# Kernel optimization log

Hardware: AMD Instinct MI355X
Metric: run time of the kernel (lower is better)

## Reference

```python
import jax, jax.numpy as jnp
import numpy as np

B, S, D = 1, 2048, 4096
N_Q, N_KV, HD = 32, 8, 128
N_REP = N_Q // N_KV
WINDOW = 1024
NEG = -1e9


def setup_inputs() -> dict:
    key = jax.random.key(0)
    ks = jax.random.split(key, 6)
    x = jax.random.normal(ks[0], (B, S, D), dtype=jnp.float32)
    # RoPE frequencies (Llama-style): theta = 10000^{-2i/HD}
    inv_freq = 1.0 / (10000.0 ** (np.arange(0, HD, 2, dtype=np.float32) / HD))
    t = np.arange(S, dtype=np.float32)
    ang = np.outer(t, inv_freq)  # [S, HD//2]
    freqs_cos = jnp.asarray(np.cos(ang), dtype=jnp.float32)
    freqs_sin = jnp.asarray(np.sin(ang), dtype=jnp.float32)
    # additive causal mask [S, S]: 0 on/below diag, -1e9 above
    mask = jnp.where(jnp.tril(jnp.ones((S, S), dtype=bool)), 0.0, NEG).astype(jnp.float32)
    scale = 0.02
    w_q = jax.random.normal(ks[1], (D, N_Q * HD), dtype=jnp.float32) * scale
    w_k = jax.random.normal(ks[2], (D, N_KV * HD), dtype=jnp.float32) * scale
    w_v = jax.random.normal(ks[3], (D, N_KV * HD), dtype=jnp.float32) * scale
    w_o = jax.random.normal(ks[4], (N_Q * HD, D), dtype=jnp.float32) * scale
    return {"x": x, "freqs_cos": freqs_cos, "freqs_sin": freqs_sin, "mask": mask,
            "w_q": w_q, "w_k": w_k, "w_v": w_v, "w_o": w_o}


def _rope(t, cos, sin):
    # t: [B, S, H, HD]; cos/sin: [S, HD//2] -> complex multiply on pairs
    tp = t.reshape(*t.shape[:-1], HD // 2, 2)
    e, o = tp[..., 0], tp[..., 1]
    c = cos[None, :, None, :]
    s = sin[None, :, None, :]
    re = e * c - o * s
    ro = e * s + o * c
    return jnp.stack([re, ro], axis=-1).reshape(t.shape)


def reference(x, freqs_cos, freqs_sin, mask, w_q, w_k, w_v, w_o):
    b, s, _ = x.shape
    xq = (x @ w_q).reshape(b, s, N_Q, HD)
    xk = (x @ w_k).reshape(b, s, N_KV, HD)
    xv = (x @ w_v).reshape(b, s, N_KV, HD)
    xq = _rope(xq, freqs_cos, freqs_sin)
    xk = _rope(xk, freqs_cos, freqs_sin)
    # GQA head repeat
    keys = jnp.repeat(xk, N_REP, axis=2)    # [b, s, N_Q, HD]
    values = jnp.repeat(xv, N_REP, axis=2)
    q = xq.transpose(0, 2, 1, 3)            # [b, h, s, hd]
    k = keys.transpose(0, 2, 1, 3)
    v = values.transpose(0, 2, 1, 3)
    scores = jnp.einsum('bhqd,bhkd->bhqk', q, k) / jnp.sqrt(jnp.float32(HD))
    scores = scores + mask[None, None, :, :]
    # sliding-window band: attend only to keys within WINDOW positions back
    idx = jnp.arange(s)
    diff = idx[:, None] - idx[None, :]
    sliding = (diff >= 0) & (diff < WINDOW)
    scores = jnp.where(sliding[None, None, :, :], scores, NEG)
    probs = jax.nn.softmax(scores, axis=-1).astype(q.dtype)
    out = jnp.einsum('bhqk,bhkd->bhqd', probs, v)
    out = out.transpose(0, 2, 1, 3).reshape(b, s, N_Q * HD)
    return out @ w_o
```

## Files before the change

### kernel.cpp

```cpp
#include <hip/hip_runtime.h>

typedef unsigned short u16;
typedef unsigned int u32;
typedef __bf16 bf16x8 __attribute__((ext_vector_type(8)));
typedef __bf16 bf16x4 __attribute__((ext_vector_type(4)));
typedef float f32x4 __attribute__((ext_vector_type(4)));

#define MFMA16(a, b, c) __builtin_amdgcn_mfma_f32_16x16x32_bf16(a, b, c, 0, 0, 0)

__device__ __forceinline__ u16 f2bf(float f) {
  u32 u = __float_as_uint(f);
  u += 0x7FFFu + ((u >> 16) & 1u);
  return (u16)(u >> 16);
}
__device__ __forceinline__ float bf2f(u16 h) {
  return __uint_as_float(((u32)h) << 16);
}

__device__ __forceinline__ void gload_lds16(const u16* g, u16* l) {
  __builtin_amdgcn_global_load_lds((__attribute__((address_space(1))) void*)g,
                                   (__attribute__((address_space(3))) void*)l,
                                   16, 0, 0);
}

__global__ __launch_bounds__(256) void cvt_x(const float* __restrict__ in,
                                             u16* __restrict__ out) {
  int i = (blockIdx.x * 256 + threadIdx.x) * 4;
  float4 v = *(const float4*)&in[i];
  ushort4 o;
  o.x = f2bf(v.x);
  o.y = f2bf(v.y);
  o.z = f2bf(v.z);
  o.w = f2bf(v.w);
  *(ushort4*)&out[i] = o;
}

__global__ __launch_bounds__(256) void tbf_f2b(const float* __restrict__ in,
                                               u16* __restrict__ out,
                                               int ldin, int ldout) {
  __shared__ float tile[64][65];
  const int t = threadIdx.x;
  const int c4 = t & 15;
  const int rb = t >> 4;
  const int r0 = blockIdx.y * 64;
  const int c0 = blockIdx.x * 64;
#pragma unroll
  for (int p = 0; p < 4; p++) {
    int r = p * 16 + rb;
    float4 v = *(const float4*)&in[(size_t)(r0 + r) * ldin + c0 + c4 * 4];
    tile[r][c4 * 4 + 0] = v.x;
    tile[r][c4 * 4 + 1] = v.y;
    tile[r][c4 * 4 + 2] = v.z;
    tile[r][c4 * 4 + 3] = v.w;
  }
  __syncthreads();
#pragma unroll
  for (int p = 0; p < 4; p++) {
    int oc = p * 16 + rb;
    ushort4 v;
    v.x = f2bf(tile[c4 * 4 + 0][oc]);
    v.y = f2bf(tile[c4 * 4 + 1][oc]);
    v.z = f2bf(tile[c4 * 4 + 2][oc]);
    v.w = f2bf(tile[c4 * 4 + 3][oc]);
    *(ushort4*)&out[(size_t)(c0 + oc) * ldout + r0 + c4 * 4] = v;
  }
}

__global__ __launch_bounds__(256) void tbf_b(const u16* __restrict__ in,
                                             u16* __restrict__ out,
                                             int ldin, int ldout) {
  __shared__ u16 tile[64][68];
  const int t = threadIdx.x;
  const int c4 = t & 15;
  const int rb = t >> 4;
  const int r0 = blockIdx.y * 64;
  const int c0 = blockIdx.x * 64;
#pragma unroll
  for (int p = 0; p < 4; p++) {
    int r = p * 16 + rb;
    ushort4 v = *(const ushort4*)&in[(size_t)(r0 + r) * ldin + c0 + c4 * 4];
    *(ushort4*)&tile[r][c4 * 4] = v;
  }
  __syncthreads();
#pragma unroll
  for (int p = 0; p < 4; p++) {
    int oc = p * 16 + rb;
    ushort4 v;
    v.x = tile[c4 * 4 + 0][oc];
    v.y = tile[c4 * 4 + 1][oc];
    v.z = tile[c4 * 4 + 2][oc];
    v.w = tile[c4 * 4 + 3][oc];
    *(ushort4*)&out[(size_t)(c0 + oc) * ldout + r0 + c4 * 4] = v;
  }
}

__global__ __launch_bounds__(256) void gemm_bt(
    const u16* __restrict__ A, const u16* __restrict__ B1,
    const u16* __restrict__ B2, const u16* __restrict__ B3,
    void* __restrict__ Cv, int K, int ldc, int n1, int n12, int f32out) {
  __shared__ __attribute__((aligned(16))) u16 AsS[128 * 32];
  __shared__ __attribute__((aligned(16))) u16 BsS[128 * 32];
  const int tid = threadIdx.x;
  const int wave = tid >> 6;
  const int lane = tid & 63;
  const int l16 = lane & 15;
  const int quad = lane >> 4;
  const int bm = blockIdx.y * 128;
  const int bn0 = blockIdx.x * 128;

  const u16* Bp;
  int bnl;
  if (bn0 < n1) { Bp = B1; bnl = bn0; }
  else if (bn0 < n12) { Bp = B2; bnl = bn0 - n1; }
  else { Bp = B3; bnl = bn0 - n12; }

  const int chunk = wave * 2;
  const int srow = chunk * 16 + (lane >> 2);
  const int skq = (lane & 3) * 8;
  const u16* gA0 = A + (size_t)(bm + srow) * K + skq;
  const u16* gB0 = Bp + (size_t)(bnl + srow) * K + skq;
  u16* lA0 = &AsS[chunk * 512];
  u16* lB0 = &BsS[chunk * 512];
  const size_t k16 = (size_t)16 * K;

  f32x4 acc[4][4];
#pragma unroll
  for (int i = 0; i < 4; i++)
#pragma unroll
    for (int j = 0; j < 4; j++) acc[i][j] = (f32x4){0.f, 0.f, 0.f, 0.f};

  const int wr = (wave >> 1) * 64;
  const int wc = (wave & 1) * 64;

  for (int k0 = 0; k0 < K; k0 += 32) {
    __syncthreads();
    gload_lds16(gA0 + k0, lA0);
    gload_lds16(gA0 + k0 + k16, lA0 + 512);
    gload_lds16(gB0 + k0, lB0);
    gload_lds16(gB0 + k0 + k16, lB0 + 512);
    __syncthreads();
    bf16x8 af[4], bfr[4];
#pragma unroll
    for (int i = 0; i < 4; i++)
      af[i] = *(const bf16x8*)&AsS[(wr + i * 16 + l16) * 32 + quad * 8];
#pragma unroll
    for (int j = 0; j < 4; j++)
      bfr[j] = *(const bf16x8*)&BsS[(wc + j * 16 + l16) * 32 + quad * 8];
#pragma unroll
    for (int i = 0; i < 4; i++)
#pragma unroll
      for (int j = 0; j < 4; j++)
        acc[i][j] = MFMA16(af[i], bfr[j], acc[i][j]);
  }
  if (f32out) {
    float* C = (float*)Cv;
#pragma unroll
    for (int i = 0; i < 4; i++)
#pragma unroll
      for (int j = 0; j < 4; j++)
#pragma unroll
        for (int r = 0; r < 4; r++) {
          int row = bm + wr + i * 16 + quad * 4 + r;
          int col = bn0 + wc + j * 16 + l16;
          C[(size_t)row * ldc + col] = acc[i][j][r];
        }
  } else {
    u16* C = (u16*)Cv;
#pragma unroll
    for (int i = 0; i < 4; i++)
#pragma unroll
      for (int j = 0; j < 4; j++)
#pragma unroll
        for (int r = 0; r < 4; r++) {
          int row = bm + wr + i * 16 + quad * 4 + r;
          int col = bn0 + wc + j * 16 + l16;
          C[(size_t)row * ldc + col] = f2bf(acc[i][j][r]);
        }
  }
}

__global__ __launch_bounds__(256) void rope_k(u16* __restrict__ qkv,
                                              const float* __restrict__ fc,
                                              const float* __restrict__ fs) {
  int idx = blockIdx.x * 256 + threadIdx.x;
  int j = idx & 63;
  int rem = idx >> 6;
  int head = rem % 40;
  int s = rem / 40;
  float c = fc[s * 64 + j];
  float sn = fs[s * 64 + j];
  int col = (head < 32) ? (head * 128 + 2 * j) : (4096 + (head - 32) * 128 + 2 * j);
  u32* p = (u32*)&qkv[(size_t)s * 6144 + col];
  u32 v = *p;
  float e = bf2f((u16)(v & 0xFFFFu));
  float o = bf2f((u16)(v >> 16));
  float re = e * c - o * sn;
  float ro = e * sn + o * c;
  *p = (u32)f2bf(re) | ((u32)f2bf(ro) << 16);
}

__global__ __launch_bounds__(256) void attn_k(const u16* __restrict__ qkv,
                                              const u16* __restrict__ vt,
                                              u16* __restrict__ outb) {
  __shared__ __attribute__((aligned(16))) u16 Kb[2][32 * 128];
  __shared__ __attribute__((aligned(16))) u16 Vb[2][128 * 32];
  __shared__ __attribute__((aligned(16))) u16 plds[4][32 * 36];
  const int h = blockIdx.x;
  const int q0 = blockIdx.y * 128;
  const int t = threadIdx.x;
  const int wave = t >> 6;
  const int lane = t & 63;
  const int l16 = lane & 15;
  const int quad = lane >> 4;
  const int hkv = h >> 2;
  const int qw = q0 + wave * 32;
  u16* myp = &plds[wave][0];

  bf16x8 qa[2][4];
#pragma unroll
  for (int i = 0; i < 2; i++)
#pragma unroll
    for (int kc = 0; kc < 4; kc++)
      qa[i][kc] = *(const bf16x8*)&qkv[(size_t)(qw + i * 16 + l16) * 6144 +
                                       h * 128 + kc * 32 + quad * 8];

  f32x4 o[2][8];
#pragma unroll
  for (int i = 0; i < 2; i++)
#pragma unroll
    for (int d = 0; d < 8; d++) o[i][d] = (f32x4){0.f, 0.f, 0.f, 0.f};
  float lloc[2][4] = {{0.f, 0.f, 0.f, 0.f}, {0.f, 0.f, 0.f, 0.f}};

  const int kb_start = (q0 - 1023 > 0 ? q0 - 1023 : 0) & ~31;
  const int kb_last = q0 + 96;
  const float sc = 0.08838834764831845f;

  const int kr0 = t >> 4, kc0s = t & 15;
  const int kr1 = (256 + t) >> 4, kc1s = t & 15;
  const int vr0 = t >> 2, vc0s = t & 3;
  const int vr1 = (256 + t) >> 2, vc1s = t & 3;
  const u16* kg = qkv + 4096 + hkv * 128;
  const u16* vg = vt + (size_t)hkv * 128 * 2048;

#define STAGE(kb_, nb_)                                                        \
  do {                                                                         \
    int kb__ = (kb_);                                                          \
    gload_lds16(&kg[(size_t)(kb__ + kr0) * 6144 + (kc0s ^ (kr0 & 15)) * 8],    \
                &Kb[nb_][t * 8]);                                              \
    gload_lds16(&kg[(size_t)(kb__ + kr1) * 6144 + (kc1s ^ (kr1 & 15)) * 8],    \
                &Kb[nb_][2048 + t * 8]);                                       \
    gload_lds16(&vg[(size_t)vr0 * 2048 + kb__ + (vc0s ^ (vr0 & 3)) * 8],       \
                &Vb[nb_][t * 8]);                                              \
    gload_lds16(&vg[(size_t)vr1 * 2048 + kb__ + (vc1s ^ (vr1 & 3)) * 8],       \
                &Vb[nb_][2048 + t * 8]);                                       \
  } while (0)

  STAGE(kb_start, 0);
  int cur = 0;

  for (int kb = kb_start; kb <= kb_last; kb += 32) {
    __syncthreads();
    if (kb + 32 <= kb_last) STAGE(kb + 32, cur ^ 1);
    const u16* kcur = &Kb[cur][0];
    const u16* vcur = &Vb[cur][0];

    f32x4 s0[2] = {(f32x4){0.f, 0.f, 0.f, 0.f}, (f32x4){0.f, 0.f, 0.f, 0.f}};
    f32x4 s1[2] = {(f32x4){0.f, 0.f, 0.f, 0.f}, (f32x4){0.f, 0.f, 0.f, 0.f}};
#pragma unroll
    for (int kc = 0; kc < 4; kc++) {
      int ch = ((kc * 4 + quad) ^ l16) * 8;
      bf16x8 b0 = *(const bf16x8*)&kcur[l16 * 128 + ch];
      bf16x8 b1 = *(const bf16x8*)&kcur[(l16 + 16) * 128 + ch];
      s0[0] = MFMA16(qa[0][kc], b0, s0[0]);
      s1[0] = MFMA16(qa[0][kc], b1, s1[0]);
      s0[1] = MFMA16(qa[1][kc], b0, s0[1]);
      s1[1] = MFMA16(qa[1][kc], b1, s1[1]);
    }

    float p0[2][4], p1[2][4];
    bool fast = (kb + 31 <= qw) && (qw + 31 - kb <= 1023);
    if (fast) {
#pragma unroll
      for (int i = 0; i < 2; i++)
#pragma unroll
        for (int r = 0; r < 4; r++) {
          p0[i][r] = __expf(s0[i][r] * sc);
          p1[i][r] = __expf(s1[i][r] * sc);
        }
    } else {
#pragma unroll
      for (int i = 0; i < 2; i++)
#pragma unroll
        for (int r = 0; r < 4; r++) {
          int row = qw + i * 16 + quad * 4 + r;
          int col0 = kb + l16;
          int col1 = col0 + 16;
          bool v0 = (col0 <= row) && (row - col0 < 1024);
          bool v1 = (col1 <= row) && (row - col1 < 1024);
          p0[i][r] = v0 ? __expf(s0[i][r] * sc) : 0.f;
          p1[i][r] = v1 ? __expf(s1[i][r] * sc) : 0.f;
        }
    }
#pragma unroll
    for (int i = 0; i < 2; i++)
#pragma unroll
      for (int r = 0; r < 4; r++) {
        lloc[i][r] += p0[i][r] + p1[i][r];
        myp[(i * 16 + quad * 4 + r) * 36 + l16] = f2bf(p0[i][r]);
        myp[(i * 16 + quad * 4 + r) * 36 + l16 + 16] = f2bf(p1[i][r]);
      }
    asm volatile("s_waitcnt lgkmcnt(0)" ::: "memory");
    bf16x8 pa[2];
#pragma unroll
    for (int i = 0; i < 2; i++) {
      bf16x4 lo = *(const bf16x4*)&myp[(i * 16 + l16) * 36 + quad * 8];
      bf16x4 hi = *(const bf16x4*)&myp[(i * 16 + l16) * 36 + quad * 8 + 4];
#pragma unroll
      for (int j = 0; j < 4; j++) {
        pa[i][j] = lo[j];
        pa[i][j + 4] = hi[j];
      }
    }
#pragma unroll
    for (int d = 0; d < 8; d++) {
      int rv = l16 + 16 * d;
      bf16x8 vb = *(const bf16x8*)&vcur[rv * 32 + ((quad ^ (l16 & 3)) * 8)];
      o[0][d] = MFMA16(pa[0], vb, o[0][d]);
      o[1][d] = MFMA16(pa[1], vb, o[1][d]);
    }
    cur ^= 1;
  }

#pragma unroll
  for (int i = 0; i < 2; i++) {
    float inv[4];
#pragma unroll
    for (int r = 0; r < 4; r++) {
      float l = lloc[i][r];
#pragma unroll
      for (int m = 8; m >= 1; m >>= 1) l += __shfl_xor(l, m, 64);
      inv[r] = 1.0f / l;
    }
#pragma unroll
    for (int d = 0; d < 8; d++)
#pragma unroll
      for (int r = 0; r < 4; r++) {
        int row = qw + i * 16 + quad * 4 + r;
        outb[(size_t)row * 4096 + h * 128 + d * 16 + l16] =
            f2bf(o[i][d][r] * inv[r]);
      }
  }
#undef STAGE
}

extern "C" void kernel_launch(void* const* d_in, const int* in_sizes, int n_in,
                              void* d_out, int out_size, void* d_ws, size_t ws_size,
                              hipStream_t stream) {
  const float* x = (const float*)d_in[0];
  const float* fc = (const float*)d_in[1];
  const float* fs = (const float*)d_in[2];
  const float* wq = (const float*)d_in[4];
  const float* wk = (const float*)d_in[5];
  const float* wv = (const float*)d_in[6];
  const float* wo = (const float*)d_in[7];
  float* outp = (float*)d_out;
  char* ws = (char*)d_ws;
  u16* xb = (u16*)(ws);
  u16* wqT = (u16*)(ws + 16777216);
  u16* wkT = (u16*)(ws + 50331648);
  u16* wvT = (u16*)(ws + 58720256);
  u16* qkvb = (u16*)(ws + 67108864);
  u16* vtb = (u16*)(ws + 92274688);
  u16* aout = (u16*)(ws + 96468992);

  cvt_x<<<8192, 256, 0, stream>>>(x, xb);
  tbf_f2b<<<dim3(64, 64), 256, 0, stream>>>(wq, wqT, 4096, 4096);
  tbf_f2b<<<dim3(16, 64), 256, 0, stream>>>(wk, wkT, 1024, 4096);
  tbf_f2b<<<dim3(16, 64), 256, 0, stream>>>(wv, wvT, 1024, 4096);
  gemm_bt<<<dim3(48, 16), 256, 0, stream>>>(xb, wqT, wkT, wvT, qkvb, 4096, 6144,
                                            4096, 5120, 0);
  rope_k<<<20480, 256, 0, stream>>>(qkvb, fc, fs);
  tbf_b<<<dim3(16, 32), 256, 0, stream>>>(qkvb + 5120, vtb, 6144, 2048);
  tbf_f2b<<<dim3(64, 64), 256, 0, stream>>>(wo, wqT, 4096, 4096);
  attn_k<<<dim3(32, 16), 256, 0, stream>>>(qkvb, vtb, aout);
  gemm_bt<<<dim3(32, 16), 256, 0, stream>>>(aout, wqT, wqT, wqT, outp, 4096,
                                            4096, 4096, 8192, 1);
}
```

Measured before the change: 538.7 us.

## Replace GEMM with 256-row double-buffered, XOR-swizzled MFMA kernel

Replaces the 128x128, K=32 single-buffered GEMM with a templated kernel using 256xBN tiles, K=64 steps, 512 threads, LDS double buffering through async global-to-LDS loads, and an XOR swizzle to avoid bank conflicts. The Q/K/V weights now sit in one contiguous transposed buffer, so the projection GEMM no longer chooses between three B pointers. It is meant to cut global traffic per MFMA and hide load latency behind compute. In exchange it uses more LDS and registers, and correctness depends on hand-tuned vmcnt waits.

Measured after the change: 507.0 us. 1.06x faster.

```diff
diff --git a/kernel.cpp b/kernel.cpp
--- a/kernel.cpp
+++ b/kernel.cpp
@@ -94,88 +94,139 @@
   }
 }
 
-__global__ __launch_bounds__(256) void gemm_bt(
-    const u16* __restrict__ A, const u16* __restrict__ B1,
-    const u16* __restrict__ B2, const u16* __restrict__ B3,
-    void* __restrict__ Cv, int K, int ldc, int n1, int n12, int f32out) {
-  __shared__ __attribute__((aligned(16))) u16 AsS[128 * 32];
-  __shared__ __attribute__((aligned(16))) u16 BsS[128 * 32];
+template <int BN, int F32OUT>
+__global__ __launch_bounds__(512, 2) void gemm256(const u16* __restrict__ A,
+                                                  const u16* __restrict__ B,
+                                                  void* __restrict__ Cv,
+                                                  int K, int ldc) {
+  constexpr int NJ = BN / 64;
+  __shared__ __attribute__((aligned(16))) u16 As[2][256 * 64];
+  __shared__ __attribute__((aligned(16))) u16 Bs[2][BN * 64];
   const int tid = threadIdx.x;
   const int wave = tid >> 6;
   const int lane = tid & 63;
   const int l16 = lane & 15;
   const int quad = lane >> 4;
-  const int bm = blockIdx.y * 128;
-  const int bn0 = blockIdx.x * 128;
-
-  const u16* Bp;
-  int bnl;
-  if (bn0 < n1) { Bp = B1; bnl = bn0; }
-  else if (bn0 < n12) { Bp = B2; bnl = bn0 - n1; }
-  else { Bp = B3; bnl = bn0 - n12; }
-
-  const int chunk = wave * 2;
-  const int srow = chunk * 16 + (lane >> 2);
-  const int skq = (lane & 3) * 8;
-  const u16* gA0 = A + (size_t)(bm + srow) * K + skq;
-  const u16* gB0 = Bp + (size_t)(bnl + srow) * K + skq;
-  u16* lA0 = &AsS[chunk * 512];
-  u16* lB0 = &BsS[chunk * 512];
-  const size_t k16 = (size_t)16 * K;
-
-  f32x4 acc[4][4];
-#pragma unroll
-  for (int i = 0; i < 4; i++)
-#pragma unroll
-    for (int j = 0; j < 4; j++) acc[i][j] = (f32x4){0.f, 0.f, 0.f, 0.f};
-
-  const int wr = (wave >> 1) * 64;
-  const int wc = (wave & 1) * 64;
-
-  for (int k0 = 0; k0 < K; k0 += 32) {
-    __syncthreads();
-    gload_lds16(gA0 + k0, lA0);
-    gload_lds16(gA0 + k0 + k16, lA0 + 512);
-    gload_lds16(gB0 + k0, lB0);
-    gload_lds16(gB0 + k0 + k16, lB0 + 512);
-    __syncthreads();
-    bf16x8 af[4], bfr[4];
-#pragma unroll
-    for (int i = 0; i < 4; i++)
-      af[i] = *(const bf16x8*)&AsS[(wr + i * 16 + l16) * 32 + quad * 8];
-#pragma unroll
-    for (int j = 0; j < 4; j++)
-      bfr[j] = *(const bf16x8*)&BsS[(wc + j * 16 + l16) * 32 + quad * 8];
-#pragma unroll
-    for (int i = 0; i < 4; i++)
-#pragma unroll
-      for (int j = 0; j < 4; j++)
-        acc[i][j] = MFMA16(af[i], bfr[j], acc[i][j]);
-  }
-  if (f32out) {
+  const int wm = wave >> 2;
+  const int wn = wave & 3;
+  const int id = blockIdx.y * gridDim.x + blockIdx.x;
+  const int bm = (id & 7) * 256;
+  const int bn0 = (id >> 3) * BN;
+
+  const u16* srcA[4];
+  const u16* srcB[NJ];
+#pragma unroll
+  for (int m = 0; m < 4; m++) {
+    int c = (wave * 4 + m) * 64 + lane;
+    int r = c >> 3;
+    int hl = (c & 7) ^ (r & 7);
+    srcA[m] = A + (size_t)(bm + r) * K + hl * 8;
+  }
+#pragma unroll
+  for (int m = 0; m < NJ; m++) {
+    int c = (wave * NJ + m) * 64 + lane;
+    int r = c >> 3;
+    int hl = (c & 7) ^ (r & 7);
+    srcB[m] = B + (size_t)(bn0 + r) * K + hl * 8;
+  }
+
+  f32x4 acc[8][NJ];
+#pragma unroll
+  for (int i = 0; i < 8; i++)
+#pragma unroll
+    for (int j = 0; j < NJ; j++) acc[i][j] = (f32x4){0.f, 0.f, 0.f, 0.f};
+
+  auto stage = [&](int nb) {
+#pragma unroll
+    for (int m = 0; m < 4; m++) {
+      gload_lds16(srcA[m], &As[nb][(size_t)((wave * 4 + m) * 64 + lane) * 8]);
+      srcA[m] += 64;
+    }
+#pragma unroll
+    for (int m = 0; m < NJ; m++) {
+      gload_lds16(srcB[m], &Bs[nb][(size_t)((wave * NJ + m) * 64 + lane) * 8]);
+      srcB[m] += 64;
+    }
+  };
+
+  stage(0);
+  const int NT = K >> 6;
+  int cur = 0;
+  for (int t = 0; t < NT; ++t) {
+    if (t + 1 < NT) {
+      stage(cur ^ 1);
+      if constexpr (NJ == 3)
+        asm volatile("s_waitcnt vmcnt(7)" ::: "memory");
+      else
+        asm volatile("s_waitcnt vmcnt(6)" ::: "memory");
+    } else {
+      asm volatile("s_waitcnt vmcnt(0)" ::: "memory");
+    }
+    __builtin_amdgcn_s_barrier();
+    __builtin_amdgcn_sched_barrier(0);
+    const u16* as = &As[cur][0];
+    const u16* bs = &Bs[cur][0];
+#pragma unroll
+    for (int ks = 0; ks < 2; ks++) {
+      bf16x8 bfr[NJ];
+#pragma unroll
+      for (int j = 0; j < NJ; j++) {
+        int r = wn * (BN / 4) + j * 16 + l16;
+        int h = (ks * 4 + quad) ^ (r & 7);
+        bfr[j] = *(const bf16x8*)&bs[r * 64 + h * 8];
+      }
+#pragma unroll
+      for (int ih = 0; ih < 2; ih++) {
+        bf16x8 afr[4];
+#pragma unroll
+        for (int i = 0; i < 4; i++) {
+          int r = wm * 128 + ih * 64 + i * 16 + l16;
+          int h = (ks * 4 + quad) ^ (r & 7);
+          afr[i] = *(const bf16x8*)&as[r * 64 + h * 8];
+        }
+        __builtin_amdgcn_s_setprio(1);
+#pragma unroll
+        for (int i = 0; i < 4; i++)
+#pragma unroll
+          for (int j = 0; j < NJ; j++)
+            acc[ih * 4 + i][j] = MFMA16(afr[i], bfr[j], acc[ih * 4 + i][j]);
+        __builtin_amdgcn_s_setprio(0);
+      }
+    }
+    __builtin_amdgcn_sched_barrier(0);
+    __builtin_amdgcn_s_barrier();
+    cur ^= 1;
+  }
+
+  const int wcol = bn0 + wn * (BN / 4);
+  if constexpr (F32OUT) {
     float* C = (float*)Cv;
 #pragma unroll
-    for (int i = 0; i < 4; i++)
-#pragma unroll
-      for (int j = 0; j < 4; j++)
-#pragma unroll
-        for (int r = 0; r < 4; r++) {
-          int row = bm + wr + i * 16 + quad * 4 + r;
-          int col = bn0 + wc + j * 16 + l16;
-          C[(size_t)row * ldc + col] = acc[i][j][r];
-        }
+    for (int ih = 0; ih < 2; ih++)
+#pragma unroll
+      for (int i = 0; i < 4; i++)
+#pragma unroll
+        for (int j = 0; j < NJ; j++)
+#pragma unroll
+          for (int r = 0; r < 4; r++) {
+            int row = bm + wm * 128 + ih * 64 + i * 16 + quad * 4 + r;
+            int col = wcol + j * 16 + l16;
+            C[(size_t)row * ldc + col] = acc[ih * 4 + i][j][r];
+          }
   } else {
     u16* C = (u16*)Cv;
 #pragma unroll
-    for (int i = 0; i < 4; i++)
-#pragma unroll
-      for (int j = 0; j < 4; j++)
-#pragma unroll
-        for (int r = 0; r < 4; r++) {
-          int row = bm + wr + i * 16 + quad * 4 + r;
-          int col = bn0 + wc + j * 16 + l16;
-          C[(size_t)row * ldc + col] = f2bf(acc[i][j][r]);
-        }
+    for (int ih = 0; ih < 2; ih++)
+#pragma unroll
+      for (int i = 0; i < 4; i++)
+#pragma unroll
+        for (int j = 0; j < NJ; j++)
+#pragma unroll
+          for (int r = 0; r < 4; r++) {
+            int row = bm + wm * 128 + ih * 64 + i * 16 + quad * 4 + r;
+            int col = wcol + j * 16 + l16;
+            C[(size_t)row * ldc + col] = f2bf(acc[ih * 4 + i][j][r]);
+          }
   }
 }
 
@@ -366,23 +417,22 @@
   float* outp = (float*)d_out;
   char* ws = (char*)d_ws;
   u16* xb = (u16*)(ws);
-  u16* wqT = (u16*)(ws + 16777216);
-  u16* wkT = (u16*)(ws + 50331648);
-  u16* wvT = (u16*)(ws + 58720256);
+  u16* wqkvT = (u16*)(ws + 16777216);
   u16* qkvb = (u16*)(ws + 67108864);
   u16* vtb = (u16*)(ws + 92274688);
   u16* aout = (u16*)(ws + 96468992);
 
   cvt_x<<<8192, 256, 0, stream>>>(x, xb);
-  tbf_f2b<<<dim3(64, 64), 256, 0, stream>>>(wq, wqT, 4096, 4096);
-  tbf_f2b<<<dim3(16, 64), 256, 0, stream>>>(wk, wkT, 1024, 4096);
-  tbf_f2b<<<dim3(16, 64), 256, 0, stream>>>(wv, wvT, 1024, 4096);
-  gemm_bt<<<dim3(48, 16), 256, 0, stream>>>(xb, wqT, wkT, wvT, qkvb, 4096, 6144,
-                                            4096, 5120, 0);
+  tbf_f2b<<<dim3(64, 64), 256, 0, stream>>>(wq, wqkvT, 4096, 4096);
+  tbf_f2b<<<dim3(16, 64), 256, 0, stream>>>(wk, wqkvT + (size_t)4096 * 4096,
+                                            1024, 4096);
+  tbf_f2b<<<dim3(16, 64), 256, 0, stream>>>(wv, wqkvT + (size_t)5120 * 4096,
+                                            1024, 4096);
+  gemm256<192, 0><<<dim3(32, 8), 512, 0, stream>>>(xb, wqkvT, qkvb, 4096, 6144);
   rope_k<<<20480, 256, 0, stream>>>(qkvb, fc, fs);
   tbf_b<<<dim3(16, 32), 256, 0, stream>>>(qkvb + 5120, vtb, 6144, 2048);
-  tbf_f2b<<<dim3(64, 64), 256, 0, stream>>>(wo, wqT, 4096, 4096);
+  tbf_f2b<<<dim3(64, 64), 256, 0, stream>>>(wo, wqkvT, 4096, 4096);
   attn_k<<<dim3(32, 16), 256, 0, stream>>>(qkvb, vtb, aout);
-  gemm_bt<<<dim3(32, 16), 256, 0, stream>>>(aout, wqT, wqT, wqT, outp, 4096,
-                                            4096, 4096, 8192, 1);
-}
+  gemm256<128, 1><<<dim3(32, 8), 512, 0, stream>>>(aout, wqkvT, outp, 4096,
+                                                   4096);
+}
```
